# Kernel optimization log

Hardware: AMD Instinct MI355X
Metric: run time of the kernel (lower is better)

Reference implementation:

```python
import jax, jax.numpy as jnp
from jax import lax
import numpy as np


def _conv(x, w, b, pad):
    y = lax.conv_general_dilated(x, w, (1, 1), [(pad, pad), (pad, pad)],
                                 dimension_numbers=('NCHW', 'OIHW', 'NCHW'))
    return y + b[None, :, None, None]


def _bn(x, g, b, eps=1e-5):
    # training-mode batchnorm (batch statistics, biased variance) like torch default
    m = jnp.mean(x, (0, 2, 3), keepdims=True)
    v = jnp.mean((x - m) ** 2, (0, 2, 3), keepdims=True)
    return g[None, :, None, None] * (x - m) * lax.rsqrt(v + eps) + b[None, :, None, None]


def _maxpool2(x):
    return lax.reduce_window(x, -jnp.inf, lax.max, (1, 1, 2, 2), (1, 1, 2, 2), 'VALID')


def _power_features(x):
    # vectorized version of the per-image FFT + radial-bin histogram mean
    B, _, H, W = x.shape
    cy, cx = H // 2, W // 2
    yy, xx = jnp.meshgrid(jnp.arange(H), jnp.arange(W), indexing='ij')
    r = jnp.sqrt((xx - cx).astype(jnp.float32) ** 2 + (yy - cy).astype(jnp.float32) ** 2)
    max_r = min(H, W) // 2
    NB = 32
    r_bins = jnp.linspace(0.0, float(max_r), NB + 1)
    # bin j covers [r_bins[j], r_bins[j+1]) exactly as the torch mask
    idx = jnp.searchsorted(r_bins, r.ravel(), side='right') - 1
    valid = (idx >= 0) & (idx < NB)
    seg = jnp.where(valid, idx, NB)  # dump out-of-range into bin NB
    counts = jax.ops.segment_sum(valid.astype(jnp.float32), seg, NB + 1)[:NB]
    ps = jnp.abs(jnp.fft.fft2(x[:, 0])) ** 2  # [B,H,W]
    psf = ps.reshape(B, -1) * valid.astype(ps.dtype)[None, :]
    sums = jax.vmap(lambda p: jax.ops.segment_sum(p, seg, NB + 1))(psf)[:, :NB]
    radial = jnp.where(counts > 0, sums / jnp.maximum(counts, 1.0), 0.0)
    return jnp.log(radial + 1e-10)  # [B,32]


def reference(x, cw1, cb1, g1, bb1, cw2, cb2, g2, bb2, cw3, cb3, g3, bb3,
              cw4, cb4, g4, bb4, pcw, pcb, pg, pbb,
              pw1, pb1, pw2, pb2, pw3, pb3,
              fw1, fb1, fw2, fb2, fw3, fb3, fw4, fb4):
    h = jax.nn.relu(_bn(_conv(x, cw1, cb1, 2), g1, bb1)); h = _maxpool2(h)
    h = jax.nn.relu(_bn(_conv(h, cw2, cb2, 2), g2, bb2)); h = _maxpool2(h)
    h = jax.nn.relu(_bn(_conv(h, cw3, cb3, 1), g3, bb3)); h = _maxpool2(h)
    h = jax.nn.relu(_bn(_conv(h, cw4, cb4, 1), g4, bb4))        # [B,256,32,32]
    p = jax.nn.relu(_bn(_conv(h, pcw, pcb, 1), pg, pbb))        # [B,128,32,32]
    # adaptive avg pool (4,4): exact 8x8 windows, stride 8
    p = lax.reduce_window(p, 0.0, lax.add, (1, 1, 8, 8), (1, 1, 8, 8), 'VALID') / 64.0
    flat = p.reshape(p.shape[0], -1)  # [B,2048]
    pf = _power_features(x)           # [B,32]
    pf = jax.nn.relu(pf @ pw1.T + pb1)
    pf = jax.nn.relu(pf @ pw2.T + pb2)
    pf = jax.nn.relu(pf @ pw3.T + pb3)  # [B,64]
    c = jnp.concatenate([flat, pf], axis=1)  # [B,2112]
    c = jax.nn.relu(c @ fw1.T + fb1)
    c = jax.nn.relu(c @ fw2.T + fb2)
    c = jax.nn.relu(c @ fw3.T + fb3)
    return c @ fw4.T + fb4  # [B,2]


def setup_inputs() -> dict:
    key = jax.random.key(0)
    ki = iter(jax.random.split(key, 40))

    def W(shape):
        fan_in = int(np.prod(shape[1:]))
        return jax.random.normal(next(ki), shape, jnp.float32) / np.sqrt(fan_in)

    d = {'x': jax.random.normal(next(ki), (16, 1, 256, 256), jnp.float32)}
    convs = [('cw1', 'cb1', 'g1', 'bb1', (32, 1, 5, 5)),
             ('cw2', 'cb2', 'g2', 'bb2', (64, 32, 5, 5)),
             ('cw3', 'cb3', 'g3', 'bb3', (128, 64, 3, 3)),
             ('cw4', 'cb4', 'g4', 'bb4', (256, 128, 3, 3)),
             ('pcw', 'pcb', 'pg', 'pbb', (128, 256, 3, 3))]
    for wn, bn, gn, ben, s in convs:
        d[wn] = W(s); d[bn] = jnp.zeros(s[0], jnp.float32)
        d[gn] = jnp.ones(s[0], jnp.float32); d[ben] = jnp.zeros(s[0], jnp.float32)
    lins = [('pw1', 'pb1', (256, 32)), ('pw2', 'pb2', (128, 256)), ('pw3', 'pb3', (64, 128)),
            ('fw1', 'fb1', (512, 2112)), ('fw2', 'fb2', (256, 512)),
            ('fw3', 'fb3', (128, 256)), ('fw4', 'fb4', (2, 128))]
    for wn, bn, s in lins:
        d[wn] = W(s); d[bn] = jnp.zeros(s[0], jnp.float32)
    return d
```

## Files before the change

### kernel.cpp

```cpp
#include <hip/hip_runtime.h>
#include <math.h>


#define PI2F 6.283185307179586f

typedef _Float16 half8 __attribute__((ext_vector_type(8)));
typedef _Float16 half4v __attribute__((ext_vector_type(4)));
typedef float f32x4 __attribute__((ext_vector_type(4)));


__device__ __forceinline__ int bitrev8(int x) {
  x = ((x & 0x0F) << 4) | ((x >> 4) & 0x0F);
  x = ((x & 0x33) << 2) | ((x >> 2) & 0x33);
  x = ((x & 0x55) << 1) | ((x >> 1) & 0x55);
  return x;
}

__global__ __launch_bounds__(64)
void fft_rows(const float* __restrict__ x, float2* __restrict__ out) {
  __shared__ float2 s[256];
  __shared__ float2 tw[128];
  int blk = blockIdx.x;
  const float* rowp = x + (size_t)blk * 256;
  int t = threadIdx.x;
  for (int i = t; i < 128; i += 64) {
    float sn, cs;
    sincosf(-(PI2F / 256.f) * (float)i, &sn, &cs);
    tw[i] = make_float2(cs, sn);
  }
  #pragma unroll
  for (int e = 0; e < 4; ++e) {
    int i = t + (e << 6);
    s[bitrev8(i)] = make_float2(rowp[i], 0.f);
  }
  __syncthreads();
  #pragma unroll
  for (int st = 1; st <= 8; ++st) {
    int half = 1 << (st - 1);
    #pragma unroll
    for (int j = 0; j < 2; ++j) {
      int bf = t + (j << 6);
      int pos = bf & (half - 1);
      int grp = bf >> (st - 1);
      int i0 = (grp << st) | pos;
      int i1 = i0 + half;
      int k = pos << (8 - st);
      float cs = tw[k].x, sn = tw[k].y;
      float2 a = s[i0], b = s[i1];
      float tr = cs * b.x - sn * b.y;
      float ti = cs * b.y + sn * b.x;
      s[i0] = make_float2(a.x + tr, a.y + ti);
      s[i1] = make_float2(a.x - tr, a.y - ti);
    }
    __syncthreads();
  }
  float2* op = out + (size_t)blk * 256;
  #pragma unroll
  for (int e = 0; e < 4; ++e) { int i = t + (e << 6); op[i] = s[i]; }
}

__device__ __forceinline__ int radial_bin(int r2) {
  int j = (int)(sqrtf((float)r2) * 0.25f);
  while ((j + 1) * (j + 1) * 16 <= r2) ++j;
  while (j > 0 && j * j * 16 > r2) --j;
  return j;
}

__global__ __launch_bounds__(256)
void fft_cols_radial_v2(const float2* __restrict__ f, float* __restrict__ radial) {
  __shared__ float2 s[8][258];
  __shared__ float2 tw[128];
  __shared__ float bins[8][32];
  int b = blockIdx.x >> 5;
  int col0 = (blockIdx.x & 31) * 8;
  int t = threadIdx.x;
  for (int i = t; i < 128; i += 256) {
    float sn, cs;
    sincosf(-(PI2F / 256.f) * (float)i, &sn, &cs);
    tw[i] = make_float2(cs, sn);
  }
  ((float*)bins)[t] = 0.f;
  for (int idx = t; idx < 2048; idx += 256) {
    int row = idx >> 3, c = idx & 7;
    s[c][bitrev8(row)] = f[(size_t)b * 65536 + row * 256 + col0 + c];
  }
  __syncthreads();
  int c = t >> 5, l = t & 31;
  float2* sc = &s[c][0];
  #pragma unroll
  for (int st = 1; st <= 8; ++st) {
    int half = 1 << (st - 1);
    #pragma unroll
    for (int j = 0; j < 4; ++j) {
      int bf = l + (j << 5);
      int pos = bf & (half - 1);
      int grp = bf >> (st - 1);
      int i0 = (grp << st) | pos;
      int i1 = i0 + half;
      int k = pos << (8 - st);
      float cs = tw[k].x, sn = tw[k].y;
      float2 a = sc[i0], bb = sc[i1];
      float tr = cs * bb.x - sn * bb.y;
      float ti = cs * bb.y + sn * bb.x;
      sc[i0] = make_float2(a.x + tr, a.y + ti);
      sc[i1] = make_float2(a.x - tr, a.y - ti);
    }
    __syncthreads();
  }
  int dx = col0 + c - 128;
  #pragma unroll
  for (int e = 0; e < 8; ++e) {
    int i = l * 8 + e;
    float2 v = sc[i];
    float ps = v.x * v.x + v.y * v.y;
    int dy = i - 128;
    int r2 = dx * dx + dy * dy;
    if (r2 < 16384) atomicAdd(&bins[c][radial_bin(r2)], ps);
  }
  __syncthreads();
  if (t < 32) {
    float s0 = bins[0][t] + bins[1][t] + bins[2][t] + bins[3][t] +
               bins[4][t] + bins[5][t] + bins[6][t] + bins[7][t];
    atomicAdd(&radial[b * 32 + t], s0);
  }
}

__device__ __forceinline__ int isqrt_(int v) {
  int r = (int)sqrtf((float)v);
  while (r * r > v) --r;
  while ((r + 1) * (r + 1) <= v) ++r;
  return r;
}

__global__ __launch_bounds__(256)
void radial_finalize_v3(const float* __restrict__ radial, float* __restrict__ pf0) {
  __shared__ int red[4];
  __shared__ int cnt_s;
  int j = blockIdx.x, t = threadIdx.x;
  int dy = t - 128;
  int lo = 16 * j * j, hi = 16 * (j + 1) * (j + 1);
  int d2 = dy * dy;
  int cnt = 0;
  int tHi = hi - 1 - d2;
  if (tHi >= 0) {
    int rHi = isqrt_(tHi);
    int nHi = min(rHi, 127) + min(rHi, 128) + 1;
    int nLo = 0;
    int tLo = lo - 1 - d2;
    if (tLo >= 0) { int rLo = isqrt_(tLo); nLo = min(rLo, 127) + min(rLo, 128) + 1; }
    cnt = nHi - nLo;
  }
  #pragma unroll
  for (int off = 32; off > 0; off >>= 1) cnt += __shfl_down(cnt, off);
  if ((t & 63) == 0) red[t >> 6] = cnt;
  __syncthreads();
  if (t == 0) cnt_s = red[0] + red[1] + red[2] + red[3];
  __syncthreads();
  if (t < 16) {
    float cf = (float)cnt_s;
    float sum = radial[t * 32 + j];
    float val = cf > 0.f ? sum / fmaxf(cf, 1.f) : 0.f;
    pf0[t * 32 + j] = logf(val + 1e-10f);
  }
}


__global__ __launch_bounds__(256)
void wtrans_all(const float* __restrict__ cw2, const float* __restrict__ cw3,
                const float* __restrict__ cw4, const float* __restrict__ pcw,
                _Float16* __restrict__ wb2, _Float16* __restrict__ wb3,
                _Float16* __restrict__ wb4, _Float16* __restrict__ wbp) {
  int blk = blockIdx.x;
  const float* src; _Float16* dst; int COUT, CIN, KK, i;
  if (blk < 200)       { src = cw2; dst = wb2; COUT = 64;  CIN = 32;  KK = 25; i = blk * 256; }
  else if (blk < 488)  { src = cw3; dst = wb3; COUT = 128; CIN = 64;  KK = 9;  i = (blk - 200) * 256; }
  else if (blk < 1640) { src = cw4; dst = wb4; COUT = 256; CIN = 128; KK = 9;  i = (blk - 488) * 256; }
  else                 { src = pcw; dst = wbp; COUT = 128; CIN = 256; KK = 9;  i = (blk - 1640) * 256; }
  i += threadIdx.x;
  if (i >= COUT * CIN * KK) return;
  int ci = i % CIN;
  int r = i / CIN;
  int co = r % COUT;
  int tap = r / COUT;
  dst[i] = (_Float16)src[((size_t)co * CIN + ci) * KK + tap];
}


__device__ __forceinline__ void load16(float* d, const float* p) {
  f32x4 v0 = *(const f32x4*)(p);
  f32x4 v1 = *(const f32x4*)(p + 4);
  f32x4 v2 = *(const f32x4*)(p + 8);
  f32x4 v3 = *(const f32x4*)(p + 12);
  #pragma unroll
  for (int e = 0; e < 4; ++e) { d[e] = v0[e]; d[4+e] = v1[e]; d[8+e] = v2[e]; d[12+e] = v3[e]; }
}

__global__ __launch_bounds__(256)
void conv1_fused(const float* __restrict__ x, const float* __restrict__ w,
                 _Float16* __restrict__ praw, size_t minoff,
                 float* __restrict__ stats) {
  __shared__ float lds[8 * 264];
  __shared__ float r1[4][32], r2[4][32];
  int t = threadIdx.x;
  int y0 = blockIdx.x * 4, n = blockIdx.y;
  const float* xp = x + (size_t)n * 65536;
  for (int i = t; i < 8 * 264; i += 256) {
    int r = i / 264, cc = i % 264;
    int gy = y0 + r - 2, gx = cc - 4;
    lds[i] = (gy >= 0 && gy < 256 && gx >= 0 && gx < 256) ? xp[gy * 256 + gx] : 0.f;
  }
  __syncthreads();
  int c = t & 31, xg = t >> 5;
  float wreg[25];
  #pragma unroll
  for (int k = 0; k < 25; ++k) wreg[k] = w[c * 25 + k];
  float s1 = 0.f, s2 = 0.f;
  for (int strip = 0; strip < 4; ++strip) {
    int px0 = xg * 8 + strip * 64;
    float f[5][16];
    #pragma unroll
    for (int rr = 0; rr < 4; ++rr) load16(f[rr], &lds[rr * 264 + px0]);
    float pmax[4], pmin[4];
    #pragma unroll
    for (int r = 0; r < 4; ++r) {
      load16(f[(r + 4) % 5], &lds[(r + 4) * 264 + px0]);
      f32x4 A = {0.f, 0.f, 0.f, 0.f}, B = {0.f, 0.f, 0.f, 0.f};
      #pragma unroll
      for (int ky = 0; ky < 5; ++ky) {
        const float* fr = f[(r + ky) % 5];
        #pragma unroll
        for (int kx = 0; kx < 5; ++kx) {
          float wv = wreg[ky * 5 + kx];
          f32x4 ia = {fr[2 + kx], fr[3 + kx], fr[4 + kx], fr[5 + kx]};
          f32x4 ib = {fr[6 + kx], fr[7 + kx], fr[8 + kx], fr[9 + kx]};
          A += wv * ia; B += wv * ib;
        }
      }
      s1 += A[0] + A[1] + A[2] + A[3] + B[0] + B[1] + B[2] + B[3];
      s2 += A[0]*A[0] + A[1]*A[1] + A[2]*A[2] + A[3]*A[3]
          + B[0]*B[0] + B[1]*B[1] + B[2]*B[2] + B[3]*B[3];
      float cm[4], cn[4];
      cm[0] = fmaxf(A[0], A[1]); cn[0] = fminf(A[0], A[1]);
      cm[1] = fmaxf(A[2], A[3]); cn[1] = fminf(A[2], A[3]);
      cm[2] = fmaxf(B[0], B[1]); cn[2] = fminf(B[0], B[1]);
      cm[3] = fmaxf(B[2], B[3]); cn[3] = fminf(B[2], B[3]);
      if ((r & 1) == 0) {
        #pragma unroll
        for (int k = 0; k < 4; ++k) { pmax[k] = cm[k]; pmin[k] = cn[k]; }
      } else {
        int prow = (y0 + r) >> 1;
        int pc0 = px0 >> 1;
        #pragma unroll
        for (int k = 0; k < 4; ++k) {
          size_t idx = (((size_t)n * 128 + prow) * 128 + pc0 + k) * 32 + c;
          praw[idx] = (_Float16)fmaxf(pmax[k], cm[k]);
          praw[minoff + idx] = (_Float16)fminf(pmin[k], cn[k]);
        }
      }
    }
  }
  s1 += __shfl_down(s1, 32);
  s2 += __shfl_down(s2, 32);
  if ((t & 63) < 32) { r1[t >> 6][t & 31] = s1; r2[t >> 6][t & 31] = s2; }
  __syncthreads();
  if (t < 32) {
    float* st = stats + (blockIdx.x & 7) * 64;
    atomicAdd(&st[t],      r1[0][t] + r1[1][t] + r1[2][t] + r1[3][t]);
    atomicAdd(&st[32 + t], r2[0][t] + r2[1][t] + r2[2][t] + r2[3][t]);
  }
}


__global__ __launch_bounds__(256)
void bn_apply(const _Float16* __restrict__ raw, size_t minoff,
              const float* __restrict__ stats, const float* __restrict__ g,
              const float* __restrict__ bb, _Float16* __restrict__ out,
              int C, int HWC, float invN) {
  __shared__ float scs[64], shs[64];
  int t = threadIdx.x, n = blockIdx.y;
  for (int c = t; c < C; c += 256) {
    float s1 = 0.f, s2 = 0.f;
    #pragma unroll
    for (int s = 0; s < 8; ++s) {
      s1 += stats[s * 2 * C + c];
      s2 += stats[s * 2 * C + C + c];
    }
    float mean = s1 * invN;
    float var  = s2 * invN - mean * mean;
    float k = g[c] / sqrtf(var + 1e-5f);
    scs[c] = k; shs[c] = bb[c] - mean * k;
  }
  __syncthreads();
  size_t basei = (size_t)n * HWC;
  int nv = HWC >> 3;
  for (int i = blockIdx.x * 256 + t; i < nv; i += gridDim.x * 256) {
    size_t off = basei + ((size_t)i << 3);
    half8 vmx = *(const half8*)(raw + off);
    half8 vmn = *(const half8*)(raw + minoff + off);
    int ch = (i << 3) & (C - 1);
    half8 o;
    #pragma unroll
    for (int j = 0; j < 8; ++j) {
      float sc = scs[ch + j];
      float xv = sc >= 0.f ? (float)vmx[j] : (float)vmn[j];
      o[j] = (_Float16)fmaxf(sc * xv + shs[ch + j], 0.f);
    }
    *(half8*)(out + off) = o;
  }
}


template <int CIN, int COUT, int H, int W, int K, int TH, int TW, int CW,
          int COT, int PT, int SLAB, int APPLY, int INPOOL, int OUTPOOL>
__global__ __launch_bounds__(256)
void conv_mfma5(const _Float16* __restrict__ in, size_t in_minoff,
                const _Float16* __restrict__ wb,
                _Float16* __restrict__ out, size_t out_minoff,
                const float* __restrict__ instats, const float* __restrict__ ing,
                const float* __restrict__ inbb, float in_invN,
                float* __restrict__ stats) {
  constexpr int P = K / 2, R = TH + 2 * P, XW = TW + 2 * P, PIX = R * XW;
  constexpr int TAPS = K * K, CSP = SLAB + 8;
  constexpr int NCC = SLAB / 32, NPH = CIN / SLAB, SUBS = SLAB / 8;
  constexpr int PW = 4 / CW, COB = CW * 16 * COT;
  static_assert(TH * TW == PW * 16 * PT, "pos tile mismatch");
  static_assert(TW == 16, "row-per-fragment requires TW=16");
  static_assert(!OUTPOOL || (PT % 2 == 0), "pool needs even PT");
  __shared__ _Float16 lds[PIX * CSP];
  __shared__ float inscs[APPLY ? CIN : 8], inshs[APPLY ? CIN : 8];
  __shared__ float sst[2][COB];
  int t = threadIdx.x;
  int lane = t & 63, wv = t >> 6;
  int lane15 = lane & 15, quad = lane >> 4;
  constexpr int WT = W / TW;
  int x0 = (blockIdx.x % WT) * TW, y0 = (blockIdx.x / WT) * TH;
  int coB = blockIdx.y * COB;
  int nb = blockIdx.z;
  int co_off = (wv % CW) * (16 * COT);
  int rowbase = (wv / CW) * PT;

  for (int i = t; i < 2 * COB; i += 256) ((float*)sst)[i] = 0.f;
  if (APPLY) {
    for (int c = t; c < CIN; c += 256) {
      float s1 = 0.f, s2 = 0.f;
      #pragma unroll
      for (int s = 0; s < 8; ++s) {
        s1 += instats[s * 2 * CIN + c];
        s2 += instats[s * 2 * CIN + CIN + c];
      }
      float mean = s1 * in_invN;
      float var  = s2 * in_invN - mean * mean;
      float k = ing[c] / sqrtf(var + 1e-5f);
      inscs[c] = k; inshs[c] = inbb[c] - mean * k;
    }
    __syncthreads();
  }

  f32x4 acc[COT][PT];
  #pragma unroll
  for (int ct = 0; ct < COT; ++ct)
    #pragma unroll
    for (int pt = 0; pt < PT; ++pt)
      #pragma unroll
      for (int e = 0; e < 4; ++e) acc[ct][pt][e] = 0.f;

  int bbase[PT];
  #pragma unroll
  for (int pt = 0; pt < PT; ++pt)
    bbase[pt] = ((rowbase + pt) * XW + lane15) * CSP + quad * 8;
  const _Float16* aptr[COT];
  #pragma unroll
  for (int ct = 0; ct < COT; ++ct)
    aptr[ct] = wb + (size_t)(coB + co_off + ct * 16 + lane15) * CIN + quad * 8;

  const size_t ibase = (size_t)nb * H * W * CIN;

  #pragma unroll
  for (int ph = 0; ph < NPH; ++ph) {
    constexpr int ITEMS = PIX * SUBS;
    for (int i = t; i < ITEMS; i += 256) {
      int sub = i % SUBS, pix = i / SUBS;
      int r = pix / XW, xx = pix % XW;
      int gy = y0 + r - P, gx = x0 + xx - P;
      int ch = ph * SLAB + sub * 8;
      half8 v;
      #pragma unroll
      for (int j = 0; j < 8; ++j) v[j] = (_Float16)0.f;
      if (gy >= 0 && gy < H && gx >= 0 && gx < W) {
        size_t off = ibase + ((size_t)gy * W + gx) * CIN + ch;
        half8 vmx = *(const half8*)(in + off);
        if (!APPLY) {
          v = vmx;
        } else if (INPOOL) {
          half8 vmn = *(const half8*)(in + in_minoff + off);
          #pragma unroll
          for (int j = 0; j < 8; ++j) {
            float sc = inscs[ch + j];
            float xv = sc >= 0.f ? (float)vmx[j] : (float)vmn[j];
            v[j] = (_Float16)fmaxf(sc * xv + inshs[ch + j], 0.f);
          }
        } else {
          #pragma unroll
          for (int j = 0; j < 8; ++j) {
            float sc = inscs[ch + j];
            v[j] = (_Float16)fmaxf(sc * (float)vmx[j] + inshs[ch + j], 0.f);
          }
        }
      }
      *(half8*)(&lds[pix * CSP + sub * 8]) = v;
    }
    __syncthreads();
    #pragma unroll
    for (int cc = 0; cc < NCC; ++cc) {
      #pragma unroll
      for (int tap = 0; tap < TAPS; ++tap) {
        int ky = tap / K, kx = tap % K;
        half8 a[COT], b[PT];
        #pragma unroll
        for (int ct = 0; ct < COT; ++ct)
          a[ct] = *(const half8*)(aptr[ct] + (size_t)tap * COUT * CIN +
                                  ph * SLAB + cc * 32);
        #pragma unroll
        for (int pt = 0; pt < PT; ++pt)
          b[pt] = *(const half8*)(&lds[bbase[pt] + (ky * XW + kx) * CSP + cc * 32]);
        #pragma unroll
        for (int ct = 0; ct < COT; ++ct)
          #pragma unroll
          for (int pt = 0; pt < PT; ++pt)
            acc[ct][pt] = __builtin_amdgcn_mfma_f32_16x16x32_f16(
                a[ct], b[pt], acc[ct][pt], 0, 0, 0);
      }
    }
    if (ph + 1 < NPH) __syncthreads();
  }

  if (OUTPOOL) {
    #pragma unroll
    for (int ct = 0; ct < COT; ++ct)
      #pragma unroll
      for (int pp = 0; pp < PT; pp += 2) {
        half4v hmax, hmin;
        #pragma unroll
        for (int e = 0; e < 4; ++e) {
          float vmx = fmaxf(acc[ct][pp][e], acc[ct][pp + 1][e]);
          float vmn = fminf(acc[ct][pp][e], acc[ct][pp + 1][e]);
          float omx = fmaxf(vmx, __shfl_xor(vmx, 1));
          float omn = fminf(vmn, __shfl_xor(vmn, 1));
          hmax[e] = (_Float16)omx; hmin[e] = (_Float16)omn;
        }
        if ((lane15 & 1) == 0) {
          int co = coB + co_off + ct * 16 + quad * 4;
          int prow = (y0 + rowbase + pp) >> 1;
          int pcol = (x0 >> 1) + (lane15 >> 1);
          size_t idx = (((size_t)nb * (H / 2) + prow) * (W / 2) + pcol) * COUT + co;
          *(half4v*)(out + idx) = hmax;
          *(half4v*)(out + out_minoff + idx) = hmin;
        }
      }
  } else {
    #pragma unroll
    for (int ct = 0; ct < COT; ++ct)
      #pragma unroll
      for (int pt = 0; pt < PT; ++pt) {
        int co = coB + co_off + ct * 16 + quad * 4;
        int y = y0 + rowbase + pt, x = x0 + lane15;
        _Float16* op = out + (((size_t)nb * H + y) * W + x) * COUT + co;
        half4v h;
        #pragma unroll
        for (int e = 0; e < 4; ++e) h[e] = (_Float16)acc[ct][pt][e];
        *(half4v*)op = h;
      }
  }

  #pragma unroll
  for (int ct = 0; ct < COT; ++ct)
    #pragma unroll
    for (int e = 0; e < 4; ++e) {
      float sv = 0.f, sq = 0.f;
      #pragma unroll
      for (int pt = 0; pt < PT; ++pt) {
        float v = acc[ct][pt][e];
        sv += v; sq += v * v;
      }
      sv += __shfl_xor(sv, 1); sq += __shfl_xor(sq, 1);
      sv += __shfl_xor(sv, 2); sq += __shfl_xor(sq, 2);
      sv += __shfl_xor(sv, 4); sq += __shfl_xor(sq, 4);
      sv += __shfl_xor(sv, 8); sq += __shfl_xor(sq, 8);
      if (lane15 == 0) {
        int cl = co_off + ct * 16 + quad * 4 + e;
        atomicAdd(&sst[0][cl], sv);
        atomicAdd(&sst[1][cl], sq);
      }
    }
  __syncthreads();
  float* st = stats + (blockIdx.x & 7) * 2 * COUT;
  for (int i = t; i < COB; i += 256) {
    atomicAdd(&st[coB + i], sst[0][i]);
    atomicAdd(&st[COUT + coB + i], sst[1][i]);
  }
}


__global__ __launch_bounds__(256)
void bn_avgpool_concat(const _Float16* __restrict__ x, const float* __restrict__ stats,
                       const float* __restrict__ g, const float* __restrict__ bb,
                       float* __restrict__ concat, float invN) {
  __shared__ float scs[128], shs[128];
  int t = threadIdx.x;
  int n = blockIdx.y;
  for (int c = t; c < 128; c += 256) {
    float s1 = 0.f, s2 = 0.f;
    #pragma unroll
    for (int s = 0; s < 8; ++s) {
      s1 += stats[s * 256 + c];
      s2 += stats[s * 256 + 128 + c];
    }
    float mean = s1 * invN;
    float var  = s2 * invN - mean * mean;
    float k = g[c] / sqrtf(var + 1e-5f);
    scs[c] = k; shs[c] = bb[c] - mean * k;
  }
  __syncthreads();
  int i = blockIdx.x * 256 + t;
  int c = i & 127, opix = i >> 7;
  int py = opix >> 2, px = opix & 3;
  float sc = scs[c], sh = shs[c];
  float s = 0.f;
  for (int yy = 0; yy < 8; ++yy)
    #pragma unroll
    for (int xx = 0; xx < 8; ++xx)
      s += fmaxf((float)x[(((size_t)n * 32 + py * 8 + yy) * 32 + px * 8 + xx) * 128 + c] * sc + sh, 0.f);
  concat[(size_t)n * 2112 + c * 16 + opix] = s * (1.f / 64.f);
}


__global__ __launch_bounds__(64)
void linear_k(const float* __restrict__ in, const float* __restrict__ w,
              const float* __restrict__ bias, float* __restrict__ out,
              int I, int in_stride, int out_stride, int relu) {
  int o = blockIdx.x, b = blockIdx.y;
  int lane = threadIdx.x;
  const float* ip = in + (size_t)b * in_stride;
  const float* wp = w + (size_t)o * I;
  float acc = 0.f;
  for (int i = lane; i < I; i += 64) acc += ip[i] * wp[i];
  #pragma unroll
  for (int off = 32; off > 0; off >>= 1) acc += __shfl_down(acc, off);
  if (lane == 0) {
    float v = acc + bias[o];
    if (relu) v = fmaxf(v, 0.f);
    out[(size_t)b * out_stride + o] = v;
  }
}

__global__ __launch_bounds__(256)
void pf_mlp(const float* __restrict__ pf0,
            const float* __restrict__ pw1, const float* __restrict__ pb1,
            const float* __restrict__ pw2, const float* __restrict__ pb2,
            const float* __restrict__ pw3, const float* __restrict__ pb3,
            float* __restrict__ concat) {
  __shared__ float a0[32], a1[256], a2[128];
  int b = blockIdx.x, t = threadIdx.x;
  if (t < 32) a0[t] = pf0[b * 32 + t];
  __syncthreads();
  {
    float s = pb1[t];
    for (int i = 0; i < 32; ++i) s += pw1[t * 32 + i] * a0[i];
    a1[t] = fmaxf(s, 0.f);
  }
  __syncthreads();
  if (t < 128) {
    float s = pb2[t];
    for (int i = 0; i < 256; ++i) s += pw2[t * 256 + i] * a1[i];
    a2[t] = fmaxf(s, 0.f);
  }
  __syncthreads();
  if (t < 64) {
    float s = pb3[t];
    for (int i = 0; i < 128; ++i) s += pw3[t * 128 + i] * a2[i];
    concat[(size_t)b * 2112 + 2048 + t] = fmaxf(s, 0.f);
  }
}

__global__ __launch_bounds__(256)
void fc_tail(const float* __restrict__ fc1o,
             const float* __restrict__ fw2, const float* __restrict__ fb2,
             const float* __restrict__ fw3, const float* __restrict__ fb3,
             const float* __restrict__ fw4, const float* __restrict__ fb4,
             float* __restrict__ out) {
  __shared__ float a1[512], a2[256], a3[128];
  int b = blockIdx.x, t = threadIdx.x;
  a1[t] = fc1o[b * 512 + t];
  a1[t + 256] = fc1o[b * 512 + t + 256];
  __syncthreads();
  {
    float s = fb2[t];
    for (int i = 0; i < 512; ++i) s += fw2[t * 512 + i] * a1[i];
    a2[t] = fmaxf(s, 0.f);
  }
  __syncthreads();
  if (t < 128) {
    float s = fb3[t];
    for (int i = 0; i < 256; ++i) s += fw3[t * 256 + i] * a2[i];
    a3[t] = fmaxf(s, 0.f);
  }
  __syncthreads();
  if (t < 2) {
    float s = fb4[t];
    for (int i = 0; i < 128; ++i) s += fw4[t * 128 + i] * a3[i];
    out[b * 2 + t] = s;
  }
}


extern "C" void kernel_launch(void* const* d_in, const int* in_sizes, int n_in,
                              void* d_out, int out_size, void* d_ws, size_t ws_size,
                              hipStream_t stream) {
  (void)in_sizes; (void)n_in; (void)out_size; (void)ws_size;
  const float* x   = (const float*)d_in[0];
  const float* cw1 = (const float*)d_in[1];
  const float* g1  = (const float*)d_in[3];
  const float* bb1 = (const float*)d_in[4];
  const float* cw2 = (const float*)d_in[5];
  const float* g2  = (const float*)d_in[7];
  const float* bb2 = (const float*)d_in[8];
  const float* cw3 = (const float*)d_in[9];
  const float* g3  = (const float*)d_in[11];
  const float* bb3 = (const float*)d_in[12];
  const float* cw4 = (const float*)d_in[13];
  const float* g4  = (const float*)d_in[15];
  const float* bb4 = (const float*)d_in[16];
  const float* pcw = (const float*)d_in[17];
  const float* pg  = (const float*)d_in[19];
  const float* pbb = (const float*)d_in[20];
  const float* pw1 = (const float*)d_in[21];
  const float* pb1 = (const float*)d_in[22];
  const float* pw2 = (const float*)d_in[23];
  const float* pb2 = (const float*)d_in[24];
  const float* pw3 = (const float*)d_in[25];
  const float* pb3 = (const float*)d_in[26];
  const float* fw1 = (const float*)d_in[27];
  const float* fb1 = (const float*)d_in[28];
  const float* fw2 = (const float*)d_in[29];
  const float* fb2 = (const float*)d_in[30];
  const float* fw3 = (const float*)d_in[31];
  const float* fb3 = (const float*)d_in[32];
  const float* fw4 = (const float*)d_in[33];
  const float* fb4 = (const float*)d_in[34];

  char* base = (char*)d_ws;
  float2*   fftbuf   = (float2*)(base + 0);
  _Float16* pool1raw = (_Float16*)(base + 0);
  _Float16* pool1app = (_Float16*)(base + 33554432);
  _Float16* pool2raw = (_Float16*)(base + 0);
  _Float16* pool2app = (_Float16*)(base + 16777216);
  _Float16* pool3raw = (_Float16*)(base + 0);
  _Float16* conv4raw = (_Float16*)(base + 8388608);
  _Float16* pconvo   = (_Float16*)(base + 16777216);
  _Float16* wb2      = (_Float16*)(base + 50331648);
  _Float16* wb3      = (_Float16*)(base + 50434048);
  _Float16* wb4      = (_Float16*)(base + 50581504);
  _Float16* wbp      = (_Float16*)(base + 51171328);
  float*    zbase    = (float*)(base + 51761152);
  float*    stats1   = zbase;
  float*    stats2   = zbase + 512;
  float*    stats3   = zbase + 1536;
  float*    stats4   = zbase + 3584;
  float*    stats5   = zbase + 7680;
  float*    radial   = zbase + 9728;
  float*    pf0      = (float*)(base + 51802112);
  float*    concat   = (float*)(base + 51804160);
  float*    fc1o     = (float*)(base + 51939328);

  hipMemsetAsync(zbase, 0, 10240 * sizeof(float), stream);

  wtrans_all<<<2792, 256, 0, stream>>>(cw2, cw3, cw4, pcw, wb2, wb3, wb4, wbp);

  fft_rows<<<4096, 64, 0, stream>>>(x, fftbuf);
  fft_cols_radial_v2<<<512, 256, 0, stream>>>(fftbuf, radial);
  radial_finalize_v3<<<32, 256, 0, stream>>>(radial, pf0);
  pf_mlp<<<16, 256, 0, stream>>>(pf0, pw1, pb1, pw2, pb2, pw3, pb3, concat);

  conv1_fused<<<dim3(64, 16), 256, 0, stream>>>(x, cw1, pool1raw, 8388608, stats1);
  bn_apply<<<dim3(128, 16), 256, 0, stream>>>(
      pool1raw, 8388608, stats1, g1, bb1, pool1app, 32, 524288, 1.f / 1048576.f);

  conv_mfma5<32, 64, 128, 128, 5, 8, 16, 2, 2, 4, 32, 0, 0, 1>
      <<<dim3(128, 1, 16), 256, 0, stream>>>(
      pool1app, 0, wb2, pool2raw, 4194304,
      nullptr, nullptr, nullptr, 0.f, stats2);
  bn_apply<<<dim3(128, 16), 256, 0, stream>>>(
      pool2raw, 4194304, stats2, g2, bb2, pool2app, 64, 262144, 1.f / 262144.f);

  conv_mfma5<64, 128, 64, 64, 3, 8, 16, 2, 4, 4, 64, 0, 0, 1>
      <<<dim3(32, 1, 16), 256, 0, stream>>>(
      pool2app, 0, wb3, pool3raw, 2097152,
      nullptr, nullptr, nullptr, 0.f, stats3);

  conv_mfma5<128, 256, 32, 32, 3, 4, 16, 2, 2, 2, 128, 1, 1, 0>
      <<<dim3(16, 4, 16), 256, 0, stream>>>(
      pool3raw, 2097152, wb4, conv4raw, 0,
      stats3, g3, bb3, 1.f / 65536.f, stats4);

  conv_mfma5<256, 128, 32, 32, 3, 4, 16, 2, 2, 2, 128, 1, 0, 0>
      <<<dim3(16, 2, 16), 256, 0, stream>>>(
      conv4raw, 0, wbp, pconvo, 0,
      stats4, g4, bb4, 1.f / 16384.f, stats5);
  bn_avgpool_concat<<<dim3(8, 16), 256, 0, stream>>>(
      pconvo, stats5, pg, pbb, concat, 1.f / 16384.f);

  linear_k<<<dim3(512, 16), 64, 0, stream>>>(concat, fw1, fb1, fc1o, 2112, 2112, 512, 1);
  fc_tail<<<16, 256, 0, stream>>>(fc1o, fw2, fb2, fw3, fb3, fw4, fb4, (float*)d_out);
}
```

Baseline: 409.6 us.

## Drop max/min pooled conv epilogue, add fused BN+pool kernels, merge radial into MLP

The max/min pooling epilogue in the MFMA conv is removed. Conv2 and conv3 now write full-resolution outputs, and new bn_applypool kernels apply batchnorm, ReLU and the 2x2 max pool afterwards. The row FFT now writes its output transposed so the column FFT reads contiguous rows, and the radial count finalize is merged into the power-feature MLP to save launches. The full-resolution conv outputs add memory traffic (four times the pooled size, no separate min buffer) and one extra kernel launch, in exchange for simpler conv epilogues.

Result: slower. 427.2 us (+4.3%).

```diff
diff --git a/kernel.cpp b/kernel.cpp
--- a/kernel.cpp
+++ b/kernel.cpp
@@ -21,6 +21,7 @@
   __shared__ float2 s[256];
   __shared__ float2 tw[128];
   int blk = blockIdx.x;
+  int b = blk >> 8, row = blk & 255;
   const float* rowp = x + (size_t)blk * 256;
   int t = threadIdx.x;
   for (int i = t; i < 128; i += 64) {
@@ -46,17 +47,20 @@
       int i1 = i0 + half;
       int k = pos << (8 - st);
       float cs = tw[k].x, sn = tw[k].y;
-      float2 a = s[i0], b = s[i1];
-      float tr = cs * b.x - sn * b.y;
-      float ti = cs * b.y + sn * b.x;
+      float2 a = s[i0], b2 = s[i1];
+      float tr = cs * b2.x - sn * b2.y;
+      float ti = cs * b2.y + sn * b2.x;
       s[i0] = make_float2(a.x + tr, a.y + ti);
       s[i1] = make_float2(a.x - tr, a.y - ti);
     }
     __syncthreads();
   }
-  float2* op = out + (size_t)blk * 256;
-  #pragma unroll
-  for (int e = 0; e < 4; ++e) { int i = t + (e << 6); op[i] = s[i]; }
+  float2* op = out + (size_t)b * 65536;
+  #pragma unroll
+  for (int e = 0; e < 4; ++e) {
+    int i = t + (e << 6);
+    op[(size_t)i * 256 + row] = s[i];
+  }
 }
 
 __device__ __forceinline__ int radial_bin(int r2) {
@@ -67,7 +71,7 @@
 }
 
 __global__ __launch_bounds__(256)
-void fft_cols_radial_v2(const float2* __restrict__ f, float* __restrict__ radial) {
+void fft_cols_radial_v3(const float2* __restrict__ f, float* __restrict__ radial) {
   __shared__ float2 s[8][258];
   __shared__ float2 tw[128];
   __shared__ float bins[8][32];
@@ -81,8 +85,8 @@
   }
   ((float*)bins)[t] = 0.f;
   for (int idx = t; idx < 2048; idx += 256) {
-    int row = idx >> 3, c = idx & 7;
-    s[c][bitrev8(row)] = f[(size_t)b * 65536 + row * 256 + col0 + c];
+    int col = idx >> 8, row = idx & 255;
+    s[col][bitrev8(row)] = f[(size_t)b * 65536 + (size_t)(col0 + col) * 256 + row];
   }
   __syncthreads();
   int c = t >> 5, l = t & 31;
@@ -133,34 +137,55 @@
 }
 
 __global__ __launch_bounds__(256)
-void radial_finalize_v3(const float* __restrict__ radial, float* __restrict__ pf0) {
-  __shared__ int red[4];
-  __shared__ int cnt_s;
-  int j = blockIdx.x, t = threadIdx.x;
-  int dy = t - 128;
+void pf_all(const float* __restrict__ radial,
+            const float* __restrict__ pw1, const float* __restrict__ pb1,
+            const float* __restrict__ pw2, const float* __restrict__ pb2,
+            const float* __restrict__ pw3, const float* __restrict__ pb3,
+            float* __restrict__ concat) {
+  __shared__ float part[8][32];
+  __shared__ float a0[32], a1[256], a2[128];
+  int b = blockIdx.x, t = threadIdx.x;
+  int j = t & 31, sub = t >> 5;
   int lo = 16 * j * j, hi = 16 * (j + 1) * (j + 1);
-  int d2 = dy * dy;
   int cnt = 0;
-  int tHi = hi - 1 - d2;
-  if (tHi >= 0) {
-    int rHi = isqrt_(tHi);
-    int nHi = min(rHi, 127) + min(rHi, 128) + 1;
-    int nLo = 0;
-    int tLo = lo - 1 - d2;
-    if (tLo >= 0) { int rLo = isqrt_(tLo); nLo = min(rLo, 127) + min(rLo, 128) + 1; }
-    cnt = nHi - nLo;
-  }
-  #pragma unroll
-  for (int off = 32; off > 0; off >>= 1) cnt += __shfl_down(cnt, off);
-  if ((t & 63) == 0) red[t >> 6] = cnt;
-  __syncthreads();
-  if (t == 0) cnt_s = red[0] + red[1] + red[2] + red[3];
-  __syncthreads();
-  if (t < 16) {
-    float cf = (float)cnt_s;
-    float sum = radial[t * 32 + j];
-    float val = cf > 0.f ? sum / fmaxf(cf, 1.f) : 0.f;
-    pf0[t * 32 + j] = logf(val + 1e-10f);
+  for (int dy = -128 + sub; dy <= 127; dy += 8) {
+    int d2 = dy * dy;
+    int tHi = hi - 1 - d2;
+    if (tHi >= 0) {
+      int rHi = isqrt_(tHi);
+      int nHi = min(rHi, 127) + min(rHi, 128) + 1;
+      int nLo = 0;
+      int tLo = lo - 1 - d2;
+      if (tLo >= 0) { int rLo = isqrt_(tLo); nLo = min(rLo, 127) + min(rLo, 128) + 1; }
+      cnt += nHi - nLo;
+    }
+  }
+  part[sub][j] = (float)cnt;
+  __syncthreads();
+  if (t < 32) {
+    float c = part[0][t] + part[1][t] + part[2][t] + part[3][t] +
+              part[4][t] + part[5][t] + part[6][t] + part[7][t];
+    float sum = radial[b * 32 + t];
+    float val = c > 0.f ? sum / fmaxf(c, 1.f) : 0.f;
+    a0[t] = logf(val + 1e-10f);
+  }
+  __syncthreads();
+  {
+    float s = pb1[t];
+    for (int i = 0; i < 32; ++i) s += pw1[t * 32 + i] * a0[i];
+    a1[t] = fmaxf(s, 0.f);
+  }
+  __syncthreads();
+  if (t < 128) {
+    float s = pb2[t];
+    for (int i = 0; i < 256; ++i) s += pw2[t * 256 + i] * a1[i];
+    a2[t] = fmaxf(s, 0.f);
+  }
+  __syncthreads();
+  if (t < 64) {
+    float s = pb3[t];
+    for (int i = 0; i < 128; ++i) s += pw3[t * 128 + i] * a2[i];
+    concat[(size_t)b * 2112 + 2048 + t] = fmaxf(s, 0.f);
   }
 }
 
@@ -271,6 +296,21 @@
 }
 
 
+__device__ __forceinline__ void bn_coeff(const float* stats, int C, int c,
+                                         float invN, const float* g,
+                                         const float* bb, float* sc, float* sh) {
+  float s1 = 0.f, s2 = 0.f;
+  #pragma unroll
+  for (int s = 0; s < 8; ++s) {
+    s1 += stats[s * 2 * C + c];
+    s2 += stats[s * 2 * C + C + c];
+  }
+  float mean = s1 * invN;
+  float var  = s2 * invN - mean * mean;
+  float k = g[c] / sqrtf(var + 1e-5f);
+  *sc = k; *sh = bb[c] - mean * k;
+}
+
 __global__ __launch_bounds__(256)
 void bn_apply(const _Float16* __restrict__ raw, size_t minoff,
               const float* __restrict__ stats, const float* __restrict__ g,
@@ -278,18 +318,7 @@
               int C, int HWC, float invN) {
   __shared__ float scs[64], shs[64];
   int t = threadIdx.x, n = blockIdx.y;
-  for (int c = t; c < C; c += 256) {
-    float s1 = 0.f, s2 = 0.f;
-    #pragma unroll
-    for (int s = 0; s < 8; ++s) {
-      s1 += stats[s * 2 * C + c];
-      s2 += stats[s * 2 * C + C + c];
-    }
-    float mean = s1 * invN;
-    float var  = s2 * invN - mean * mean;
-    float k = g[c] / sqrtf(var + 1e-5f);
-    scs[c] = k; shs[c] = bb[c] - mean * k;
-  }
+  for (int c = t; c < C; c += 256) bn_coeff(stats, C, c, invN, g, bb, &scs[c], &shs[c]);
   __syncthreads();
   size_t basei = (size_t)n * HWC;
   int nv = HWC >> 3;
@@ -309,13 +338,50 @@
   }
 }
 
+template <int C>
+__global__ __launch_bounds__(256)
+void bn_applypool(const _Float16* __restrict__ raw, const float* __restrict__ stats,
+                  const float* __restrict__ g, const float* __restrict__ bb,
+                  _Float16* __restrict__ out, int H, int W, float invN) {
+  constexpr int CT = C / 8;
+  __shared__ float scs[C], shs[C];
+  int t = threadIdx.x, n = blockIdx.y;
+  for (int c = t; c < C; c += 256) bn_coeff(stats, C, c, invN, g, bb, &scs[c], &shs[c]);
+  __syncthreads();
+  int W2 = W >> 1, H2 = H >> 1;
+  int total = H2 * W2 * CT;
+  const _Float16* xp = raw + (size_t)n * H * W * C;
+  _Float16* op = out + (size_t)n * H2 * W2 * C;
+  for (int i = blockIdx.x * 256 + t; i < total; i += gridDim.x * 256) {
+    int cb = (i % CT) * 8;
+    int pp = i / CT;
+    int py = pp / W2, px = pp % W2;
+    const _Float16* p00 = xp + ((size_t)(2 * py) * W + 2 * px) * C + cb;
+    half8 v00 = *(const half8*)(p00);
+    half8 v01 = *(const half8*)(p00 + C);
+    half8 v10 = *(const half8*)(p00 + (size_t)W * C);
+    half8 v11 = *(const half8*)(p00 + (size_t)W * C + C);
+    half8 o;
+    #pragma unroll
+    for (int j = 0; j < 8; ++j) {
+      float sc = scs[cb + j], sh = shs[cb + j];
+      float a = fmaxf(sc * (float)v00[j] + sh, 0.f);
+      float b = fmaxf(sc * (float)v01[j] + sh, 0.f);
+      float d = fmaxf(sc * (float)v10[j] + sh, 0.f);
+      float e = fmaxf(sc * (float)v11[j] + sh, 0.f);
+      o[j] = (_Float16)fmaxf(fmaxf(a, b), fmaxf(d, e));
+    }
+    *(half8*)(op + (size_t)pp * C + cb) = o;
+  }
+}
+
 
 template <int CIN, int COUT, int H, int W, int K, int TH, int TW, int CW,
-          int COT, int PT, int SLAB, int APPLY, int INPOOL, int OUTPOOL>
-__global__ __launch_bounds__(256)
-void conv_mfma5(const _Float16* __restrict__ in, size_t in_minoff,
+          int COT, int PT, int SLAB, int APPLY>
+__global__ __launch_bounds__(256)
+void conv_mfma5(const _Float16* __restrict__ in,
                 const _Float16* __restrict__ wb,
-                _Float16* __restrict__ out, size_t out_minoff,
+                _Float16* __restrict__ out,
                 const float* __restrict__ instats, const float* __restrict__ ing,
                 const float* __restrict__ inbb, float in_invN,
                 float* __restrict__ stats) {
@@ -325,7 +391,6 @@
   constexpr int PW = 4 / CW, COB = CW * 16 * COT;
   static_assert(TH * TW == PW * 16 * PT, "pos tile mismatch");
   static_assert(TW == 16, "row-per-fragment requires TW=16");
-  static_assert(!OUTPOOL || (PT % 2 == 0), "pool needs even PT");
   __shared__ _Float16 lds[PIX * CSP];
   __shared__ float inscs[APPLY ? CIN : 8], inshs[APPLY ? CIN : 8];
   __shared__ float sst[2][COB];
@@ -341,18 +406,8 @@
 
   for (int i = t; i < 2 * COB; i += 256) ((float*)sst)[i] = 0.f;
   if (APPLY) {
-    for (int c = t; c < CIN; c += 256) {
-      float s1 = 0.f, s2 = 0.f;
-      #pragma unroll
-      for (int s = 0; s < 8; ++s) {
-        s1 += instats[s * 2 * CIN + c];
-        s2 += instats[s * 2 * CIN + CIN + c];
-      }
-      float mean = s1 * in_invN;
-      float var  = s2 * in_invN - mean * mean;
-      float k = ing[c] / sqrtf(var + 1e-5f);
-      inscs[c] = k; inshs[c] = inbb[c] - mean * k;
-    }
+    for (int c = t; c < CIN; c += 256)
+      bn_coeff(instats, CIN, c, in_invN, ing, inbb, &inscs[c], &inshs[c]);
     __syncthreads();
   }
 
@@ -391,14 +446,6 @@
         half8 vmx = *(const half8*)(in + off);
         if (!APPLY) {
           v = vmx;
-        } else if (INPOOL) {
-          half8 vmn = *(const half8*)(in + in_minoff + off);
-          #pragma unroll
-          for (int j = 0; j < 8; ++j) {
-            float sc = inscs[ch + j];
-            float xv = sc >= 0.f ? (float)vmx[j] : (float)vmn[j];
-            v[j] = (_Float16)fmaxf(sc * xv + inshs[ch + j], 0.f);
-          }
         } else {
           #pragma unroll
           for (int j = 0; j < 8; ++j) {
@@ -434,43 +481,18 @@
     if (ph + 1 < NPH) __syncthreads();
   }
 
-  if (OUTPOOL) {
-    #pragma unroll
-    for (int ct = 0; ct < COT; ++ct)
+  #pragma unroll
+  for (int ct = 0; ct < COT; ++ct)
+    #pragma unroll
+    for (int pt = 0; pt < PT; ++pt) {
+      int co = coB + co_off + ct * 16 + quad * 4;
+      int y = y0 + rowbase + pt, x = x0 + lane15;
+      _Float16* op = out + (((size_t)nb * H + y) * W + x) * COUT + co;
+      half4v h;
       #pragma unroll
-      for (int pp = 0; pp < PT; pp += 2) {
-        half4v hmax, hmin;
-        #pragma unroll
-        for (int e = 0; e < 4; ++e) {
-          float vmx = fmaxf(acc[ct][pp][e], acc[ct][pp + 1][e]);
-          float vmn = fminf(acc[ct][pp][e], acc[ct][pp + 1][e]);
-          float omx = fmaxf(vmx, __shfl_xor(vmx, 1));
-          float omn = fminf(vmn, __shfl_xor(vmn, 1));
-          hmax[e] = (_Float16)omx; hmin[e] = (_Float16)omn;
-        }
-        if ((lane15 & 1) == 0) {
-          int co = coB + co_off + ct * 16 + quad * 4;
-          int prow = (y0 + rowbase + pp) >> 1;
-          int pcol = (x0 >> 1) + (lane15 >> 1);
-          size_t idx = (((size_t)nb * (H / 2) + prow) * (W / 2) + pcol) * COUT + co;
-          *(half4v*)(out + idx) = hmax;
-          *(half4v*)(out + out_minoff + idx) = hmin;
-        }
-      }
-  } else {
-    #pragma unroll
-    for (int ct = 0; ct < COT; ++ct)
-      #pragma unroll
-      for (int pt = 0; pt < PT; ++pt) {
-        int co = coB + co_off + ct * 16 + quad * 4;
-        int y = y0 + rowbase + pt, x = x0 + lane15;
-        _Float16* op = out + (((size_t)nb * H + y) * W + x) * COUT + co;
-        half4v h;
-        #pragma unroll
-        for (int e = 0; e < 4; ++e) h[e] = (_Float16)acc[ct][pt][e];
-        *(half4v*)op = h;
-      }
-  }
+      for (int e = 0; e < 4; ++e) h[e] = (_Float16)acc[ct][pt][e];
+      *(half4v*)op = h;
+    }
 
   #pragma unroll
   for (int ct = 0; ct < COT; ++ct)
@@ -508,18 +530,7 @@
   __shared__ float scs[128], shs[128];
   int t = threadIdx.x;
   int n = blockIdx.y;
-  for (int c = t; c < 128; c += 256) {
-    float s1 = 0.f, s2 = 0.f;
-    #pragma unroll
-    for (int s = 0; s < 8; ++s) {
-      s1 += stats[s * 256 + c];
-      s2 += stats[s * 256 + 128 + c];
-    }
-    float mean = s1 * invN;
-    float var  = s2 * invN - mean * mean;
-    float k = g[c] / sqrtf(var + 1e-5f);
-    scs[c] = k; shs[c] = bb[c] - mean * k;
-  }
+  for (int c = t; c < 128; c += 256) bn_coeff(stats, 128, c, invN, g, bb, &scs[c], &shs[c]);
   __syncthreads();
   int i = blockIdx.x * 256 + t;
   int c = i & 127, opix = i >> 7;
@@ -550,35 +561,6 @@
     float v = acc + bias[o];
     if (relu) v = fmaxf(v, 0.f);
     out[(size_t)b * out_stride + o] = v;
-  }
-}
-
-__global__ __launch_bounds__(256)
-void pf_mlp(const float* __restrict__ pf0,
-            const float* __restrict__ pw1, const float* __restrict__ pb1,
-            const float* __restrict__ pw2, const float* __restrict__ pb2,
-            const float* __restrict__ pw3, const float* __restrict__ pb3,
-            float* __restrict__ concat) {
-  __shared__ float a0[32], a1[256], a2[128];
-  int b = blockIdx.x, t = threadIdx.x;
-  if (t < 32) a0[t] = pf0[b * 32 + t];
-  __syncthreads();
-  {
-    float s = pb1[t];
-    for (int i = 0; i < 32; ++i) s += pw1[t * 32 + i] * a0[i];
-    a1[t] = fmaxf(s, 0.f);
-  }
-  __syncthreads();
-  if (t < 128) {
-    float s = pb2[t];
-    for (int i = 0; i < 256; ++i) s += pw2[t * 256 + i] * a1[i];
-    a2[t] = fmaxf(s, 0.f);
-  }
-  __syncthreads();
-  if (t < 64) {
-    float s = pb3[t];
-    for (int i = 0; i < 128; ++i) s += pw3[t * 128 + i] * a2[i];
-    concat[(size_t)b * 2112 + 2048 + t] = fmaxf(s, 0.f);
   }
 }
 
@@ -651,12 +633,13 @@
   char* base = (char*)d_ws;
   float2*   fftbuf   = (float2*)(base + 0);
   _Float16* pool1raw = (_Float16*)(base + 0);
+  _Float16* conv2o   = (_Float16*)(base + 0);
+  _Float16* conv3o   = (_Float16*)(base + 0);
+  _Float16* conv4raw = (_Float16*)(base + 0);
+  _Float16* pconvo   = (_Float16*)(base + 8388608);
   _Float16* pool1app = (_Float16*)(base + 33554432);
-  _Float16* pool2raw = (_Float16*)(base + 0);
-  _Float16* pool2app = (_Float16*)(base + 16777216);
-  _Float16* pool3raw = (_Float16*)(base + 0);
-  _Float16* conv4raw = (_Float16*)(base + 8388608);
-  _Float16* pconvo   = (_Float16*)(base + 16777216);
+  _Float16* pool2app = (_Float16*)(base + 33554432);
+  _Float16* pool3app = (_Float16*)(base + 33554432);
   _Float16* wb2      = (_Float16*)(base + 50331648);
   _Float16* wb3      = (_Float16*)(base + 50434048);
   _Float16* wb4      = (_Float16*)(base + 50581504);
@@ -668,7 +651,6 @@
   float*    stats4   = zbase + 3584;
   float*    stats5   = zbase + 7680;
   float*    radial   = zbase + 9728;
-  float*    pf0      = (float*)(base + 51802112);
   float*    concat   = (float*)(base + 51804160);
   float*    fc1o     = (float*)(base + 51939328);
 
@@ -677,35 +659,32 @@
   wtrans_all<<<2792, 256, 0, stream>>>(cw2, cw3, cw4, pcw, wb2, wb3, wb4, wbp);
 
   fft_rows<<<4096, 64, 0, stream>>>(x, fftbuf);
-  fft_cols_radial_v2<<<512, 256, 0, stream>>>(fftbuf, radial);
-  radial_finalize_v3<<<32, 256, 0, stream>>>(radial, pf0);
-  pf_mlp<<<16, 256, 0, stream>>>(pf0, pw1, pb1, pw2, pb2, pw3, pb3, concat);
+  fft_cols_radial_v3<<<512, 256, 0, stream>>>(fftbuf, radial);
+  pf_all<<<16, 256, 0, stream>>>(radial, pw1, pb1, pw2, pb2, pw3, pb3, concat);
 
   conv1_fused<<<dim3(64, 16), 256, 0, stream>>>(x, cw1, pool1raw, 8388608, stats1);
   bn_apply<<<dim3(128, 16), 256, 0, stream>>>(
       pool1raw, 8388608, stats1, g1, bb1, pool1app, 32, 524288, 1.f / 1048576.f);
 
-  conv_mfma5<32, 64, 128, 128, 5, 8, 16, 2, 2, 4, 32, 0, 0, 1>
+  conv_mfma5<32, 64, 128, 128, 5, 8, 16, 2, 2, 4, 32, 0>
       <<<dim3(128, 1, 16), 256, 0, stream>>>(
-      pool1app, 0, wb2, pool2raw, 4194304,
-      nullptr, nullptr, nullptr, 0.f, stats2);
-  bn_apply<<<dim3(128, 16), 256, 0, stream>>>(
-      pool2raw, 4194304, stats2, g2, bb2, pool2app, 64, 262144, 1.f / 262144.f);
-
-  conv_mfma5<64, 128, 64, 64, 3, 8, 16, 2, 4, 4, 64, 0, 0, 1>
+      pool1app, wb2, conv2o, nullptr, nullptr, nullptr, 0.f, stats2);
+  bn_applypool<64><<<dim3(32, 16), 256, 0, stream>>>(
+      conv2o, stats2, g2, bb2, pool2app, 128, 128, 1.f / 262144.f);
+
+  conv_mfma5<64, 128, 64, 64, 3, 8, 16, 2, 4, 4, 64, 0>
       <<<dim3(32, 1, 16), 256, 0, stream>>>(
-      pool2app, 0, wb3, pool3raw, 2097152,
-      nullptr, nullptr, nullptr, 0.f, stats3);
-
-  conv_mfma5<128, 256, 32, 32, 3, 4, 16, 2, 2, 2, 128, 1, 1, 0>
+      pool2app, wb3, conv3o, nullptr, nullptr, nullptr, 0.f, stats3);
+  bn_applypool<128><<<dim3(16, 16), 256, 0, stream>>>(
+      conv3o, stats3, g3, bb3, pool3app, 64, 64, 1.f / 65536.f);
+
+  conv_mfma5<128, 256, 32, 32, 3, 4, 16, 2, 2, 2, 128, 0>
       <<<dim3(16, 4, 16), 256, 0, stream>>>(
-      pool3raw, 2097152, wb4, conv4raw, 0,
-      stats3, g3, bb3, 1.f / 65536.f, stats4);
-
-  conv_mfma5<256, 128, 32, 32, 3, 4, 16, 2, 2, 2, 128, 1, 0, 0>
+      pool3app, wb4, conv4raw, nullptr, nullptr, nullptr, 0.f, stats4);
+
+  conv_mfma5<256, 128, 32, 32, 3, 4, 16, 2, 2, 2, 128, 1>
       <<<dim3(16, 2, 16), 256, 0, stream>>>(
-      conv4raw, 0, wbp, pconvo, 0,
-      stats4, g4, bb4, 1.f / 16384.f, stats5);
+      conv4raw, wbp, pconvo, stats4, g4, bb4, 1.f / 16384.f, stats5);
   bn_avgpool_concat<<<dim3(8, 16), 256, 0, stream>>>(
       pconvo, stats5, pg, pbb, concat, 1.f / 16384.f);
 
```
